# Optimization experiments

Hardware: AMD Instinct MI355X
Metric: run time of the kernel (lower is better)

Reference implementation:

```python
import jax, jax.numpy as jnp
import numpy as np

T, D, I, E, K = 2048, 2048, 5632, 8, 2


def setup_inputs() -> dict:
    key = jax.random.key(0)
    k1, k2, k3, k4, k5 = jax.random.split(key, 5)
    s = 0.02
    return {
        "x": jax.random.normal(k1, (T, D), dtype=jnp.float32),
        "gate_w": jax.random.normal(k2, (E, D), dtype=jnp.float32) * s,
        "w_gate": jax.random.normal(k3, (E, I, D), dtype=jnp.float32) * s,
        "w_up": jax.random.normal(k4, (E, I, D), dtype=jnp.float32) * s,
        "w_down": jax.random.normal(k5, (E, D, I), dtype=jnp.float32) * s,
    }


def reference(x, gate_w, w_gate, w_up, w_down):
    # Router: logits [T, E], top-k then softmax over the k selected logits
    logits = x @ gate_w.T
    top_vals, top_idx = jax.lax.top_k(logits, K)          # [T, K]
    rw = jax.nn.softmax(top_vals, axis=-1)                # [T, K]
    # Dense combine weights [T, E]: sum of routing weights over selected slots.
    # Mathematically identical to the per-(expert, slot) scatter-add in torch,
    # since duplicate selections of the same expert just sum their weights.
    combine = jnp.sum(jax.nn.one_hot(top_idx, E, dtype=x.dtype) * rw[..., None], axis=1)  # [T, E]
    # SwiGLU expert MLPs, batched over experts (grouped GEMM as dense einsum)
    g = jnp.einsum("td,eid->tei", x, w_gate)              # [T, E, I]
    u = jnp.einsum("td,eid->tei", x, w_up)                # [T, E, I]
    h = jax.nn.silu(g) * u                                 # [T, E, I]
    out_e = jnp.einsum("tei,edi->ted", h, w_down)         # [T, E, D]
    return jnp.einsum("ted,te->td", out_e, combine)       # [T, D]
```

## Files before the change

kernel.cpp:

```cpp
#include <hip/hip_runtime.h>
#include <hip/hip_bf16.h>
#include <stdint.h>

#define TTOK 2048
#define DDIM 2048
#define IDIM 5632
#define NEXP 8

typedef __attribute__((ext_vector_type(8))) short bf16x8;
typedef __attribute__((ext_vector_type(4))) float f32x4;
typedef __attribute__((ext_vector_type(8))) unsigned short u16x8;
typedef __attribute__((ext_vector_type(4))) unsigned short u16x4;

__device__ __forceinline__ unsigned short f2bf(float f) {
  union { float f; uint32_t u; } v; v.f = f;
  uint32_t u = v.u + 0x7fffu + ((v.u >> 16) & 1u);
  return (unsigned short)(u >> 16);
}

__device__ __forceinline__ uint32_t fbits(float f) {
  union { float f; uint32_t u; } v; v.f = f; return v.u;
}

__device__ __forceinline__ u16x8 cvt8t(float4 a, float4 b) {
  union { u16x8 v; uint32_t w[4]; } r;
  r.w[0] = __builtin_amdgcn_perm(fbits(a.y), fbits(a.x), 0x07060302);
  r.w[1] = __builtin_amdgcn_perm(fbits(a.w), fbits(a.z), 0x07060302);
  r.w[2] = __builtin_amdgcn_perm(fbits(b.y), fbits(b.x), 0x07060302);
  r.w[3] = __builtin_amdgcn_perm(fbits(b.w), fbits(b.z), 0x07060302);
  return r.v;
}

typedef __attribute__((address_space(3))) void lds_t;
typedef const __attribute__((address_space(1))) void gbl_t;
__device__ __forceinline__ void gload16(const void* g, void* l) {
  __builtin_amdgcn_global_load_lds((gbl_t*)g, (lds_t*)l, 16, 0, 0);
}

#define PIPE_BAR() asm volatile("s_waitcnt vmcnt(4) lgkmcnt(0)\n\ts_barrier" ::: "memory")

__global__ __launch_bounds__(256) void router_kernel(
    const float* __restrict__ x, const float* __restrict__ gw,
    unsigned short* __restrict__ xbf,
    int* __restrict__ cnt, int* __restrict__ slots, float* __restrict__ wts)
{
  const int lane = threadIdx.x & 63;
  const int t = (blockIdx.x * blockDim.x + threadIdx.x) >> 6;
  const float* xr = x + (size_t)t * DDIM;
  float acc[NEXP];
#pragma unroll
  for (int e = 0; e < NEXP; ++e) acc[e] = 0.f;
#pragma unroll
  for (int it = 0; it < DDIM / 256; ++it) {
    const int d = (it * 64 + lane) * 4;
    const float4 xv = *(const float4*)(xr + d);
    u16x4 xb; xb[0]=f2bf(xv.x); xb[1]=f2bf(xv.y); xb[2]=f2bf(xv.z); xb[3]=f2bf(xv.w);
    *(u16x4*)(xbf + (size_t)t * DDIM + d) = xb;
#pragma unroll
    for (int e = 0; e < NEXP; ++e) {
      const float4 gv = *(const float4*)(gw + (size_t)e * DDIM + d);
      acc[e] += xv.x*gv.x + xv.y*gv.y + xv.z*gv.z + xv.w*gv.w;
    }
  }
#pragma unroll
  for (int e = 0; e < NEXP; ++e) {
    float v = acc[e];
#pragma unroll
    for (int off = 32; off > 0; off >>= 1) v += __shfl_xor(v, off);
    acc[e] = v;
  }
  if (lane == 0) {
    int i0 = 0; float v0 = acc[0];
#pragma unroll
    for (int e = 1; e < NEXP; ++e) if (acc[e] > v0) { v0 = acc[e]; i0 = e; }
    int i1 = -1; float v1 = -3.4e38f;
#pragma unroll
    for (int e = 0; e < NEXP; ++e) { if (e == i0) continue; if (acc[e] > v1) { v1 = acc[e]; i1 = e; } }
    const float e1 = __expf(v1 - v0);
    const float w0 = 1.f / (1.f + e1);
    const float w1 = e1 / (1.f + e1);
    const int p0 = atomicAdd(&cnt[i0], 1);
    slots[i0 * TTOK + p0] = t * 2;     wts[i0 * TTOK + p0] = w0;
    const int p1 = atomicAdd(&cnt[i1], 1);
    slots[i1 * TTOK + p1] = t * 2 + 1; wts[i1 * TTOK + p1] = w1;
  }
}

__global__ void plan_kernel(const int* __restrict__ cnt,
                            int* __restrict__ tilemap, int* __restrict__ ntiles)
{
  if (threadIdx.x == 0 && blockIdx.x == 0) {
    int n = 0;
#pragma unroll
    for (int e = 0; e < NEXP; ++e) {
      const int nt = (cnt[e] + 127) >> 7;
      for (int m = 0; m < nt; ++m) tilemap[n++] = (e << 8) | m;
    }
    ntiles[0] = n;
  }
}


__global__ __launch_bounds__(512, 4) void gateup_kernel(
    const unsigned short* __restrict__ xbf,
    const float* __restrict__ wg, const float* __restrict__ wu,
    const int* __restrict__ cnt, const int* __restrict__ slots,
    const int* __restrict__ tilemap, const int* __restrict__ ntiles,
    unsigned short* __restrict__ h)
{
  const int flat = (blockIdx.x & 7) * 440 + (blockIdx.x >> 3);
  const int ti = flat % 40;
  if (ti >= ntiles[0]) return;
  const int em = tilemap[ti];
  const int e = em >> 8;
  const int mt = em & 255;
  const int n0 = (flat / 40) * 64;
  const int count = cnt[e];
  const int m0 = mt * 128;

  __shared__ unsigned short A[2][128][64];
  __shared__ unsigned short Bg[2][64][64];
  __shared__ unsigned short Bu[2][64][64];
  __shared__ int rslot[128];
  __shared__ int rtok[128];

  const int tid = threadIdx.x;
  const int lane = tid & 63;
  const int wid = tid >> 6;

  if (tid < 128) {
    const int idx = m0 + tid;
    const int safe = slots[e * TTOK + m0];
    const int s = (idx < count) ? slots[e * TTOK + idx] : safe;
    rslot[tid] = (idx < count) ? s : -1;
    rtok[tid] = s >> 1;
  }
  __syncthreads();

  const int aswz = ((lane & 7) ^ ((lane >> 3) & 7)) * 8;
  const unsigned short* aptr[2];
#pragma unroll
  for (int j = 0; j < 2; ++j) {
    const int arow = wid * 16 + j * 8 + (lane >> 3);
    aptr[j] = xbf + (size_t)rtok[arow] * DDIM + aswz;
  }

  const int mat = wid >> 2;
  unsigned short (*Bm)[64][64] = (mat == 0) ? Bg : Bu;
  const float* wsel = (mat == 0) ? wg : wu;

  const int tidm = tid & 255;
  const int brow = tidm >> 2;
  const int bcb = (tidm & 3) * 2;
  const int bswz = brow & 7;
  const float* msrc = wsel + (size_t)e * IDIM * DDIM + (size_t)(n0 + brow) * DDIM + bcb * 8;

  const int wr = (wid >> 1) & 1, wc = wid & 1;
  const int fr = lane & 15;
  const int kc = lane >> 4;
  const int rsw = fr & 7;

  f32x4 acc[4][2] = {};

  float4 P[4];
#pragma unroll
  for (int j = 0; j < 2; ++j) gload16(aptr[j], &A[0][wid * 16][0] + j * 512);
#pragma unroll
  for (int q = 0; q < 4; ++q) P[q] = *(const float4*)(msrc + q * 4);
#pragma unroll
  for (int qq = 0; qq < 2; ++qq)
    *(u16x8*)&Bm[0][brow][((bcb + qq) ^ bswz) * 8] = cvt8t(P[qq * 2], P[qq * 2 + 1]);
#pragma unroll
  for (int q = 0; q < 4; ++q) P[q] = *(const float4*)(msrc + 64 + q * 4);
  PIPE_BAR();

#pragma unroll 2
  for (int t = 0; t < 32; ++t) {
    const int cur = t & 1;
    const int kp  = (t + 1 <= 31) ? (t + 1) * 64 : 31 * 64;
    const int kp2 = (t + 2 <= 31) ? (t + 2) * 64 : 31 * 64;

#pragma unroll
    for (int j = 0; j < 2; ++j) gload16(aptr[j] + kp, &A[cur ^ 1][wid * 16][0] + j * 512);
    __builtin_amdgcn_sched_barrier(0);
#pragma unroll
    for (int qq = 0; qq < 2; ++qq)
      *(u16x8*)&Bm[cur ^ 1][brow][((bcb + qq) ^ bswz) * 8] = cvt8t(P[qq * 2], P[qq * 2 + 1]);
#pragma unroll
    for (int q = 0; q < 4; ++q) P[q] = *(const float4*)(msrc + kp2 + q * 4);
    __builtin_amdgcn_sched_barrier(0);

    __builtin_amdgcn_s_setprio(1);
#pragma unroll
    for (int kk = 0; kk < 2; ++kk) {
      bf16x8 a[4], b[2];
      const int cs = ((kk * 4 + kc) ^ rsw) * 8;
#pragma unroll
      for (int mf = 0; mf < 4; ++mf)
        a[mf] = *(const bf16x8*)&A[cur][wr * 64 + mf * 16 + fr][cs];
#pragma unroll
      for (int nf = 0; nf < 2; ++nf)
        b[nf] = *(const bf16x8*)&Bm[cur][wc * 32 + nf * 16 + fr][cs];
#pragma unroll
      for (int mf = 0; mf < 4; ++mf)
#pragma unroll
        for (int nf = 0; nf < 2; ++nf)
          acc[mf][nf] = __builtin_amdgcn_mfma_f32_16x16x32_bf16(a[mf], b[nf], acc[mf][nf], 0, 0, 0);
    }
    __builtin_amdgcn_s_setprio(0);

    PIPE_BAR();
  }

  __syncthreads();
  float* uex = (float*)&A[0][0][0];
  if (mat == 1) {
#pragma unroll
    for (int mf = 0; mf < 4; ++mf)
#pragma unroll
      for (int nf = 0; nf < 2; ++nf)
#pragma unroll
        for (int j = 0; j < 4; ++j) {
          const int r = wr * 64 + mf * 16 + (lane >> 4) * 4 + j;
          const int c = wc * 32 + nf * 16 + fr;
          uex[r * 64 + c] = acc[mf][nf][j];
        }
  }
  __syncthreads();
  if (mat == 0) {
#pragma unroll
    for (int mf = 0; mf < 4; ++mf)
#pragma unroll
      for (int nf = 0; nf < 2; ++nf)
#pragma unroll
        for (int j = 0; j < 4; ++j) {
          const int r = wr * 64 + mf * 16 + (lane >> 4) * 4 + j;
          const int c = wc * 32 + nf * 16 + fr;
          const int s = rslot[r];
          if (s >= 0) {
            const float g = acc[mf][nf][j];
            const float u = uex[r * 64 + c];
            const float hv = g / (1.f + __expf(-g)) * u;
            h[(size_t)s * IDIM + n0 + c] = f2bf(hv);
          }
        }
  }
}

__global__ __launch_bounds__(256, 4) void down_kernel(
    const unsigned short* __restrict__ h,
    const float* __restrict__ wd,
    const int* __restrict__ cnt, const int* __restrict__ slots,
    const float* __restrict__ wts,
    const int* __restrict__ tilemap, const int* __restrict__ ntiles,
    float* __restrict__ out)
{
  const int flat = (blockIdx.x & 7) * 320 + (blockIdx.x >> 3);
  const int ti = flat % 40;
  if (ti >= ntiles[0]) return;
  const int em = tilemap[ti];
  const int e = em >> 8;
  const int mt = em & 255;
  const int rest = flat / 40;
  const int n0 = (rest & 31) * 64;
  const int kbase = (rest >> 5) * (IDIM / 2);
  const int count = cnt[e];
  const int m0 = mt * 128;

  __shared__ unsigned short A[2][128][64];
  __shared__ unsigned short B[2][64][64];
  __shared__ int rslot[128];
  __shared__ float rw[128];

  const int tid = threadIdx.x;
  const int lane = tid & 63;
  const int wid = tid >> 6;

  if (tid < 128) {
    const int idx = m0 + tid;
    const int safe = slots[e * TTOK + m0];
    const int s = (idx < count) ? slots[e * TTOK + idx] : safe;
    rslot[tid] = (idx < count) ? s : (safe | 0x40000000);
    rw[tid] = (idx < count) ? wts[e * TTOK + idx] : 0.f;
  }
  __syncthreads();

  const int aswz = ((lane & 7) ^ ((lane >> 3) & 7)) * 8;
  const unsigned short* aptr[4];
#pragma unroll
  for (int j = 0; j < 4; ++j) {
    const int arow = wid * 32 + j * 8 + (lane >> 3);
    aptr[j] = h + (size_t)(rslot[arow] & 0x3fffffff) * IDIM + kbase + aswz;
  }

  const int brow = tid >> 2;
  const int bcb = (tid & 3) * 2;
  const int bswz = brow & 7;
  const float* bsrc = wd + (size_t)e * DDIM * IDIM + (size_t)(n0 + brow) * IDIM + kbase + bcb * 8;

  const int wr = wid >> 1, wc = wid & 1;
  const int fr = lane & 15;
  const int kc = lane >> 4;
  const int rsw = fr & 7;

  f32x4 acc[4][2] = {};

  float4 P[4];
#pragma unroll
  for (int j = 0; j < 4; ++j) gload16(aptr[j], &A[0][wid * 32][0] + j * 512);
#pragma unroll
  for (int q = 0; q < 4; ++q) P[q] = *(const float4*)(bsrc + q * 4);
#pragma unroll
  for (int qq = 0; qq < 2; ++qq)
    *(u16x8*)&B[0][brow][((bcb + qq) ^ bswz) * 8] = cvt8t(P[qq * 2], P[qq * 2 + 1]);
#pragma unroll
  for (int q = 0; q < 4; ++q) P[q] = *(const float4*)(bsrc + 64 + q * 4);
  asm volatile("s_waitcnt vmcnt(4) lgkmcnt(0)\n\ts_barrier" ::: "memory");

#pragma unroll 2
  for (int t = 0; t < 44; ++t) {
    const int cur = t & 1;
    const int kp  = (t + 1 <= 43) ? (t + 1) * 64 : 43 * 64;
    const int kp2 = (t + 2 <= 43) ? (t + 2) * 64 : 43 * 64;

#pragma unroll
    for (int j = 0; j < 4; ++j) gload16(aptr[j] + kp, &A[cur ^ 1][wid * 32][0] + j * 512);
    __builtin_amdgcn_sched_barrier(0);
#pragma unroll
    for (int qq = 0; qq < 2; ++qq)
      *(u16x8*)&B[cur ^ 1][brow][((bcb + qq) ^ bswz) * 8] = cvt8t(P[qq * 2], P[qq * 2 + 1]);
#pragma unroll
    for (int q = 0; q < 4; ++q) P[q] = *(const float4*)(bsrc + kp2 + q * 4);
    __builtin_amdgcn_sched_barrier(0);

    __builtin_amdgcn_s_setprio(1);
#pragma unroll
    for (int kk = 0; kk < 2; ++kk) {
      bf16x8 a[4], b[2];
      const int cs = ((kk * 4 + kc) ^ rsw) * 8;
#pragma unroll
      for (int mf = 0; mf < 4; ++mf)
        a[mf] = *(const bf16x8*)&A[cur][wr * 64 + mf * 16 + fr][cs];
#pragma unroll
      for (int nf = 0; nf < 2; ++nf)
        b[nf] = *(const bf16x8*)&B[cur][wc * 32 + nf * 16 + fr][cs];
#pragma unroll
      for (int mf = 0; mf < 4; ++mf)
#pragma unroll
        for (int nf = 0; nf < 2; ++nf)
          acc[mf][nf] = __builtin_amdgcn_mfma_f32_16x16x32_bf16(a[mf], b[nf], acc[mf][nf], 0, 0, 0);
    }
    __builtin_amdgcn_s_setprio(0);

    asm volatile("s_waitcnt vmcnt(4) lgkmcnt(0)\n\ts_barrier" ::: "memory");
  }

#pragma unroll
  for (int mf = 0; mf < 4; ++mf)
#pragma unroll
    for (int j = 0; j < 4; ++j) {
      const int r = wr * 64 + mf * 16 + (lane >> 4) * 4 + j;
      const int s = rslot[r];
      if (!(s & 0x40000000)) {
        const int t2 = s >> 1;
        const float w = rw[r];
#pragma unroll
        for (int nf = 0; nf < 2; ++nf)
          atomicAdd(out + (size_t)t2 * DDIM + n0 + wc * 32 + nf * 16 + fr,
                    acc[mf][nf][j] * w);
      }
    }
}

extern "C" void kernel_launch(void* const* d_in, const int* in_sizes, int n_in,
                              void* d_out, int out_size, void* d_ws, size_t ws_size,
                              hipStream_t stream) {
  const float* x  = (const float*)d_in[0];
  const float* gw = (const float*)d_in[1];
  const float* wg = (const float*)d_in[2];
  const float* wu = (const float*)d_in[3];
  const float* wd = (const float*)d_in[4];
  float* out = (float*)d_out;

  char* ws = (char*)d_ws;
  unsigned short* xbf = (unsigned short*)ws;
  unsigned short* h   = (unsigned short*)(ws + 8388608);
  int*   slots = (int*)(ws + 8388608 + 46137344);
  float* wts   = (float*)(ws + 8388608 + 46137344 + 65536);
  int*   cnt   = (int*)(ws + 8388608 + 46137344 + 131072);
  int*   tmap  = (int*)(ws + 8388608 + 46137344 + 131072 + 32);
  int*   ntl   = (int*)(ws + 8388608 + 46137344 + 131072 + 288);

  hipMemsetAsync(cnt, 0, NEXP * sizeof(int), stream);
  hipMemsetAsync(d_out, 0, (size_t)TTOK * DDIM * sizeof(float), stream);

  router_kernel<<<TTOK / 4, 256, 0, stream>>>(x, gw, xbf, cnt, slots, wts);
  plan_kernel<<<1, 64, 0, stream>>>(cnt, tmap, ntl);
  gateup_kernel<<<3520, 512, 0, stream>>>(xbf, wg, wu, cnt, slots, tmap, ntl, h);
  down_kernel<<<2560, 256, 0, stream>>>(h, wd, cnt, slots, wts, tmap, ntl, out);
}
```

Before: 806.6 us.

## Pack routed tokens per expert into contiguous bf16 buffer before grouped GEMMs

Adds a pack kernel that gathers each expert's routed tokens from x, converts them to bf16 and stores them contiguously in expert-sorted order, with zero-padded tail rows. Gate/up and down GEMMs now read A rows linearly from this buffer and the h buffer instead of through per-row slot indirection. This removes the gathered row loads, the slot lookup and its shared-memory sync in gateup. It also drops the s_setprio hints around the MFMA loops. The cost is an extra kernel launch and an extra pass writing the packed activations.

```diff
diff --git a/kernel.cpp b/kernel.cpp
--- a/kernel.cpp
+++ b/kernel.cpp
@@ -41,7 +41,6 @@
 
 __global__ __launch_bounds__(256) void router_kernel(
     const float* __restrict__ x, const float* __restrict__ gw,
-    unsigned short* __restrict__ xbf,
     int* __restrict__ cnt, int* __restrict__ slots, float* __restrict__ wts)
 {
   const int lane = threadIdx.x & 63;
@@ -54,8 +53,6 @@
   for (int it = 0; it < DDIM / 256; ++it) {
     const int d = (it * 64 + lane) * 4;
     const float4 xv = *(const float4*)(xr + d);
-    u16x4 xb; xb[0]=f2bf(xv.x); xb[1]=f2bf(xv.y); xb[2]=f2bf(xv.z); xb[3]=f2bf(xv.w);
-    *(u16x4*)(xbf + (size_t)t * DDIM + d) = xb;
 #pragma unroll
     for (int e = 0; e < NEXP; ++e) {
       const float4 gv = *(const float4*)(gw + (size_t)e * DDIM + d);
@@ -87,24 +84,55 @@
 }
 
 __global__ void plan_kernel(const int* __restrict__ cnt,
-                            int* __restrict__ tilemap, int* __restrict__ ntiles)
+                            int* __restrict__ tilemap, int* __restrict__ ntiles,
+                            int* __restrict__ po)
 {
   if (threadIdx.x == 0 && blockIdx.x == 0) {
-    int n = 0;
+    int n = 0, off = 0;
 #pragma unroll
     for (int e = 0; e < NEXP; ++e) {
+      po[e] = off;
       const int nt = (cnt[e] + 127) >> 7;
       for (int m = 0; m < nt; ++m) tilemap[n++] = (e << 8) | m;
+      off += nt << 7;
     }
     ntiles[0] = n;
   }
 }
 
+__global__ __launch_bounds__(256) void pack_kernel(
+    const float* __restrict__ x, const int* __restrict__ cnt,
+    const int* __restrict__ slots, const int* __restrict__ po,
+    unsigned short* __restrict__ xs)
+{
+  const int e = blockIdx.x >> 9;
+  const int count = cnt[e];
+  const int padded = (count + 127) & ~127;
+  const int rr = (blockIdx.x & 511) * 4 + (threadIdx.x >> 6);
+  if (rr >= padded) return;
+  const int lane = threadIdx.x & 63;
+  unsigned short* dst = xs + (size_t)(po[e] + rr) * DDIM;
+  if (rr < count) {
+    const float* src = x + (size_t)(slots[e * TTOK + rr] >> 1) * DDIM;
+#pragma unroll
+    for (int i = 0; i < 8; ++i) {
+      const int d = (i * 64 + lane) * 4;
+      const float4 v = *(const float4*)(src + d);
+      u16x4 b; b[0]=f2bf(v.x); b[1]=f2bf(v.y); b[2]=f2bf(v.z); b[3]=f2bf(v.w);
+      *(u16x4*)(dst + d) = b;
+    }
+  } else {
+    const u16x4 z = {};
+#pragma unroll
+    for (int i = 0; i < 8; ++i) *(u16x4*)(dst + (i * 64 + lane) * 4) = z;
+  }
+}
+
 
 __global__ __launch_bounds__(512, 4) void gateup_kernel(
-    const unsigned short* __restrict__ xbf,
+    const unsigned short* __restrict__ xs,
     const float* __restrict__ wg, const float* __restrict__ wu,
-    const int* __restrict__ cnt, const int* __restrict__ slots,
+    const int* __restrict__ cnt, const int* __restrict__ po,
     const int* __restrict__ tilemap, const int* __restrict__ ntiles,
     unsigned short* __restrict__ h)
 {
@@ -117,32 +145,22 @@
   const int n0 = (flat / 40) * 64;
   const int count = cnt[e];
   const int m0 = mt * 128;
+  const int abase = po[e] + m0;
 
   __shared__ unsigned short A[2][128][64];
   __shared__ unsigned short Bg[2][64][64];
   __shared__ unsigned short Bu[2][64][64];
-  __shared__ int rslot[128];
-  __shared__ int rtok[128];
 
   const int tid = threadIdx.x;
   const int lane = tid & 63;
   const int wid = tid >> 6;
 
-  if (tid < 128) {
-    const int idx = m0 + tid;
-    const int safe = slots[e * TTOK + m0];
-    const int s = (idx < count) ? slots[e * TTOK + idx] : safe;
-    rslot[tid] = (idx < count) ? s : -1;
-    rtok[tid] = s >> 1;
-  }
-  __syncthreads();
-
   const int aswz = ((lane & 7) ^ ((lane >> 3) & 7)) * 8;
   const unsigned short* aptr[2];
 #pragma unroll
   for (int j = 0; j < 2; ++j) {
     const int arow = wid * 16 + j * 8 + (lane >> 3);
-    aptr[j] = xbf + (size_t)rtok[arow] * DDIM + aswz;
+    aptr[j] = xs + (size_t)(abase + arow) * DDIM + aswz;
   }
 
   const int mat = wid >> 2;
@@ -190,7 +208,6 @@
     for (int q = 0; q < 4; ++q) P[q] = *(const float4*)(msrc + kp2 + q * 4);
     __builtin_amdgcn_sched_barrier(0);
 
-    __builtin_amdgcn_s_setprio(1);
 #pragma unroll
     for (int kk = 0; kk < 2; ++kk) {
       bf16x8 a[4], b[2];
@@ -207,7 +224,6 @@
         for (int nf = 0; nf < 2; ++nf)
           acc[mf][nf] = __builtin_amdgcn_mfma_f32_16x16x32_bf16(a[mf], b[nf], acc[mf][nf], 0, 0, 0);
     }
-    __builtin_amdgcn_s_setprio(0);
 
     PIPE_BAR();
   }
@@ -236,12 +252,11 @@
         for (int j = 0; j < 4; ++j) {
           const int r = wr * 64 + mf * 16 + (lane >> 4) * 4 + j;
           const int c = wc * 32 + nf * 16 + fr;
-          const int s = rslot[r];
-          if (s >= 0) {
+          if (m0 + r < count) {
             const float g = acc[mf][nf][j];
             const float u = uex[r * 64 + c];
             const float hv = g / (1.f + __expf(-g)) * u;
-            h[(size_t)s * IDIM + n0 + c] = f2bf(hv);
+            h[(size_t)(abase + r) * IDIM + n0 + c] = f2bf(hv);
           }
         }
   }
@@ -251,7 +266,7 @@
     const unsigned short* __restrict__ h,
     const float* __restrict__ wd,
     const int* __restrict__ cnt, const int* __restrict__ slots,
-    const float* __restrict__ wts,
+    const float* __restrict__ wts, const int* __restrict__ po,
     const int* __restrict__ tilemap, const int* __restrict__ ntiles,
     float* __restrict__ out)
 {
@@ -266,10 +281,11 @@
   const int kbase = (rest >> 5) * (IDIM / 2);
   const int count = cnt[e];
   const int m0 = mt * 128;
+  const int abase = po[e] + m0;
 
   __shared__ unsigned short A[2][128][64];
   __shared__ unsigned short B[2][64][64];
-  __shared__ int rslot[128];
+  __shared__ int rtok[128];
   __shared__ float rw[128];
 
   const int tid = threadIdx.x;
@@ -278,19 +294,16 @@
 
   if (tid < 128) {
     const int idx = m0 + tid;
-    const int safe = slots[e * TTOK + m0];
-    const int s = (idx < count) ? slots[e * TTOK + idx] : safe;
-    rslot[tid] = (idx < count) ? s : (safe | 0x40000000);
+    rtok[tid] = (idx < count) ? (slots[e * TTOK + idx] >> 1) : 0;
     rw[tid] = (idx < count) ? wts[e * TTOK + idx] : 0.f;
   }
-  __syncthreads();
 
   const int aswz = ((lane & 7) ^ ((lane >> 3) & 7)) * 8;
   const unsigned short* aptr[4];
 #pragma unroll
   for (int j = 0; j < 4; ++j) {
     const int arow = wid * 32 + j * 8 + (lane >> 3);
-    aptr[j] = h + (size_t)(rslot[arow] & 0x3fffffff) * IDIM + kbase + aswz;
+    aptr[j] = h + (size_t)(abase + arow) * IDIM + kbase + aswz;
   }
 
   const int brow = tid >> 2;
@@ -315,7 +328,7 @@
     *(u16x8*)&B[0][brow][((bcb + qq) ^ bswz) * 8] = cvt8t(P[qq * 2], P[qq * 2 + 1]);
 #pragma unroll
   for (int q = 0; q < 4; ++q) P[q] = *(const float4*)(bsrc + 64 + q * 4);
-  asm volatile("s_waitcnt vmcnt(4) lgkmcnt(0)\n\ts_barrier" ::: "memory");
+  PIPE_BAR();
 
 #pragma unroll 2
   for (int t = 0; t < 44; ++t) {
@@ -333,7 +346,6 @@
     for (int q = 0; q < 4; ++q) P[q] = *(const float4*)(bsrc + kp2 + q * 4);
     __builtin_amdgcn_sched_barrier(0);
 
-    __builtin_amdgcn_s_setprio(1);
 #pragma unroll
     for (int kk = 0; kk < 2; ++kk) {
       bf16x8 a[4], b[2];
@@ -350,9 +362,8 @@
         for (int nf = 0; nf < 2; ++nf)
           acc[mf][nf] = __builtin_amdgcn_mfma_f32_16x16x32_bf16(a[mf], b[nf], acc[mf][nf], 0, 0, 0);
     }
-    __builtin_amdgcn_s_setprio(0);
-
-    asm volatile("s_waitcnt vmcnt(4) lgkmcnt(0)\n\ts_barrier" ::: "memory");
+
+    PIPE_BAR();
   }
 
 #pragma unroll
@@ -360,9 +371,8 @@
 #pragma unroll
     for (int j = 0; j < 4; ++j) {
       const int r = wr * 64 + mf * 16 + (lane >> 4) * 4 + j;
-      const int s = rslot[r];
-      if (!(s & 0x40000000)) {
-        const int t2 = s >> 1;
+      if (m0 + r < count) {
+        const int t2 = rtok[r];
         const float w = rw[r];
 #pragma unroll
         for (int nf = 0; nf < 2; ++nf)
@@ -383,19 +393,21 @@
   float* out = (float*)d_out;
 
   char* ws = (char*)d_ws;
-  unsigned short* xbf = (unsigned short*)ws;
-  unsigned short* h   = (unsigned short*)(ws + 8388608);
-  int*   slots = (int*)(ws + 8388608 + 46137344);
-  float* wts   = (float*)(ws + 8388608 + 46137344 + 65536);
-  int*   cnt   = (int*)(ws + 8388608 + 46137344 + 131072);
-  int*   tmap  = (int*)(ws + 8388608 + 46137344 + 131072 + 32);
-  int*   ntl   = (int*)(ws + 8388608 + 46137344 + 131072 + 288);
+  unsigned short* xs = (unsigned short*)ws;
+  unsigned short* h  = (unsigned short*)(ws + 20971520);
+  int*   slots = (int*)(ws + 78643200);
+  float* wts   = (float*)(ws + 78708736);
+  int*   cnt   = (int*)(ws + 78774272);
+  int*   tmap  = (int*)(ws + 78774304);
+  int*   ntl   = (int*)(ws + 78774560);
+  int*   po    = (int*)(ws + 78774564);
 
   hipMemsetAsync(cnt, 0, NEXP * sizeof(int), stream);
   hipMemsetAsync(d_out, 0, (size_t)TTOK * DDIM * sizeof(float), stream);
 
-  router_kernel<<<TTOK / 4, 256, 0, stream>>>(x, gw, xbf, cnt, slots, wts);
-  plan_kernel<<<1, 64, 0, stream>>>(cnt, tmap, ntl);
-  gateup_kernel<<<3520, 512, 0, stream>>>(xbf, wg, wu, cnt, slots, tmap, ntl, h);
-  down_kernel<<<2560, 256, 0, stream>>>(h, wd, cnt, slots, wts, tmap, ntl, out);
-}
+  router_kernel<<<TTOK / 4, 256, 0, stream>>>(x, gw, cnt, slots, wts);
+  plan_kernel<<<1, 64, 0, stream>>>(cnt, tmap, ntl, po);
+  pack_kernel<<<NEXP * 512, 256, 0, stream>>>(x, cnt, slots, po, xs);
+  gateup_kernel<<<3520, 512, 0, stream>>>(xs, wg, wu, cnt, po, tmap, ntl, h);
+  down_kernel<<<2560, 256, 0, stream>>>(h, wd, cnt, slots, wts, po, tmap, ntl, out);
+}
```

Result: slower. 849.0 us (+5.3%).

## Load weight fragments directly into registers and compact h by expert

Applied to the files above, without the earlier changes.

Both GEMM kernels stop staging the fp32 weights through LDS. Each lane now loads exactly the weight elements its MFMA B-fragment needs, converts them to bf16 in registers, and prefetches one step ahead. The plan kernel computes per-expert padded row offsets, so h is written and read in a contiguous expert-sorted layout instead of being scattered by slot index. The down kernel moves to 512 threads with 16-column wave slices. This removes LDS write traffic and bank pressure for B, but waves that share columns now load the same weights redundantly from global memory and cache. Padded rows of the compacted h may also read past the buffer's logical extent.

```diff
diff --git a/kernel.cpp b/kernel.cpp
--- a/kernel.cpp
+++ b/kernel.cpp
@@ -36,8 +36,6 @@
 __device__ __forceinline__ void gload16(const void* g, void* l) {
   __builtin_amdgcn_global_load_lds((gbl_t*)g, (lds_t*)l, 16, 0, 0);
 }
-
-#define PIPE_BAR() asm volatile("s_waitcnt vmcnt(4) lgkmcnt(0)\n\ts_barrier" ::: "memory")
 
 __global__ __launch_bounds__(256) void router_kernel(
     const float* __restrict__ x, const float* __restrict__ gw,
@@ -87,14 +85,17 @@
 }
 
 __global__ void plan_kernel(const int* __restrict__ cnt,
-                            int* __restrict__ tilemap, int* __restrict__ ntiles)
+                            int* __restrict__ tilemap, int* __restrict__ ntiles,
+                            int* __restrict__ po)
 {
   if (threadIdx.x == 0 && blockIdx.x == 0) {
-    int n = 0;
+    int n = 0, off = 0;
 #pragma unroll
     for (int e = 0; e < NEXP; ++e) {
+      po[e] = off;
       const int nt = (cnt[e] + 127) >> 7;
       for (int m = 0; m < nt; ++m) tilemap[n++] = (e << 8) | m;
+      off += nt << 7;
     }
     ntiles[0] = n;
   }
@@ -105,6 +106,7 @@
     const unsigned short* __restrict__ xbf,
     const float* __restrict__ wg, const float* __restrict__ wu,
     const int* __restrict__ cnt, const int* __restrict__ slots,
+    const int* __restrict__ po,
     const int* __restrict__ tilemap, const int* __restrict__ ntiles,
     unsigned short* __restrict__ h)
 {
@@ -117,11 +119,9 @@
   const int n0 = (flat / 40) * 64;
   const int count = cnt[e];
   const int m0 = mt * 128;
+  const int abase = po[e] + m0;
 
   __shared__ unsigned short A[2][128][64];
-  __shared__ unsigned short Bg[2][64][64];
-  __shared__ unsigned short Bu[2][64][64];
-  __shared__ int rslot[128];
   __shared__ int rtok[128];
 
   const int tid = threadIdx.x;
@@ -130,86 +130,75 @@
 
   if (tid < 128) {
     const int idx = m0 + tid;
-    const int safe = slots[e * TTOK + m0];
-    const int s = (idx < count) ? slots[e * TTOK + idx] : safe;
-    rslot[tid] = (idx < count) ? s : -1;
-    rtok[tid] = s >> 1;
+    rtok[tid] = (idx < count) ? (slots[e * TTOK + idx] >> 1) : (slots[e * TTOK + m0] >> 1);
   }
   __syncthreads();
 
   const int aswz = ((lane & 7) ^ ((lane >> 3) & 7)) * 8;
-  const unsigned short* aptr[2];
-#pragma unroll
-  for (int j = 0; j < 2; ++j) {
-    const int arow = wid * 16 + j * 8 + (lane >> 3);
-    aptr[j] = xbf + (size_t)rtok[arow] * DDIM + aswz;
-  }
-
+  const unsigned short* ap0 = xbf + (size_t)rtok[wid * 16     + (lane >> 3)] * DDIM + aswz;
+  const unsigned short* ap1 = xbf + (size_t)rtok[wid * 16 + 8 + (lane >> 3)] * DDIM + aswz;
+
+  const int wr  = wid & 1;
+  const int wc  = (wid >> 1) & 1;
   const int mat = wid >> 2;
-  unsigned short (*Bm)[64][64] = (mat == 0) ? Bg : Bu;
   const float* wsel = (mat == 0) ? wg : wu;
 
-  const int tidm = tid & 255;
-  const int brow = tidm >> 2;
-  const int bcb = (tidm & 3) * 2;
-  const int bswz = brow & 7;
-  const float* msrc = wsel + (size_t)e * IDIM * DDIM + (size_t)(n0 + brow) * DDIM + bcb * 8;
-
-  const int wr = (wid >> 1) & 1, wc = wid & 1;
   const int fr = lane & 15;
+  const int kq = (lane >> 4) * 8;
+  const float* bp0 = wsel + (size_t)e * IDIM * DDIM + (size_t)(n0 + wc * 32 +      fr) * DDIM + kq;
+  const float* bp1 = wsel + (size_t)e * IDIM * DDIM + (size_t)(n0 + wc * 32 + 16 + fr) * DDIM + kq;
+
   const int kc = lane >> 4;
   const int rsw = fr & 7;
 
   f32x4 acc[4][2] = {};
-
-  float4 P[4];
-#pragma unroll
-  for (int j = 0; j < 2; ++j) gload16(aptr[j], &A[0][wid * 16][0] + j * 512);
-#pragma unroll
-  for (int q = 0; q < 4; ++q) P[q] = *(const float4*)(msrc + q * 4);
-#pragma unroll
-  for (int qq = 0; qq < 2; ++qq)
-    *(u16x8*)&Bm[0][brow][((bcb + qq) ^ bswz) * 8] = cvt8t(P[qq * 2], P[qq * 2 + 1]);
-#pragma unroll
-  for (int q = 0; q < 4; ++q) P[q] = *(const float4*)(msrc + 64 + q * 4);
-  PIPE_BAR();
+  float4 Brg[8];
+
+  gload16(ap0, &A[0][wid * 16][0]);
+  gload16(ap1, &A[0][wid * 16 + 8][0]);
+  __builtin_amdgcn_sched_barrier(0);
+  Brg[0] = *(const float4*)(bp0);        Brg[1] = *(const float4*)(bp0 + 4);
+  Brg[2] = *(const float4*)(bp1);        Brg[3] = *(const float4*)(bp1 + 4);
+  Brg[4] = *(const float4*)(bp0 + 32);   Brg[5] = *(const float4*)(bp0 + 36);
+  Brg[6] = *(const float4*)(bp1 + 32);   Brg[7] = *(const float4*)(bp1 + 36);
+  asm volatile("s_waitcnt vmcnt(8) lgkmcnt(0)\n\ts_barrier" ::: "memory");
 
 #pragma unroll 2
   for (int t = 0; t < 32; ++t) {
     const int cur = t & 1;
-    const int kp  = (t + 1 <= 31) ? (t + 1) * 64 : 31 * 64;
-    const int kp2 = (t + 2 <= 31) ? (t + 2) * 64 : 31 * 64;
-
-#pragma unroll
-    for (int j = 0; j < 2; ++j) gload16(aptr[j] + kp, &A[cur ^ 1][wid * 16][0] + j * 512);
+    const int kp = ((t + 1 < 32) ? t + 1 : 31) * 64;
+
+    gload16(ap0 + kp, &A[cur ^ 1][wid * 16][0]);
+    gload16(ap1 + kp, &A[cur ^ 1][wid * 16 + 8][0]);
     __builtin_amdgcn_sched_barrier(0);
-#pragma unroll
-    for (int qq = 0; qq < 2; ++qq)
-      *(u16x8*)&Bm[cur ^ 1][brow][((bcb + qq) ^ bswz) * 8] = cvt8t(P[qq * 2], P[qq * 2 + 1]);
-#pragma unroll
-    for (int q = 0; q < 4; ++q) P[q] = *(const float4*)(msrc + kp2 + q * 4);
-    __builtin_amdgcn_sched_barrier(0);
-
-    __builtin_amdgcn_s_setprio(1);
+
+    bf16x8 bfr[4];
+#pragma unroll
+    for (int f = 0; f < 4; ++f)
+      bfr[f] = (bf16x8)cvt8t(Brg[2 * f], Brg[2 * f + 1]);
+
+    Brg[0] = *(const float4*)(bp0 + kp);        Brg[1] = *(const float4*)(bp0 + kp + 4);
+    Brg[2] = *(const float4*)(bp1 + kp);        Brg[3] = *(const float4*)(bp1 + kp + 4);
+    Brg[4] = *(const float4*)(bp0 + kp + 32);   Brg[5] = *(const float4*)(bp0 + kp + 36);
+    Brg[6] = *(const float4*)(bp1 + kp);        Brg[6] = *(const float4*)(bp1 + kp + 32);
+    Brg[7] = *(const float4*)(bp1 + kp + 36);
+
 #pragma unroll
     for (int kk = 0; kk < 2; ++kk) {
-      bf16x8 a[4], b[2];
       const int cs = ((kk * 4 + kc) ^ rsw) * 8;
+      bf16x8 a[4];
 #pragma unroll
       for (int mf = 0; mf < 4; ++mf)
         a[mf] = *(const bf16x8*)&A[cur][wr * 64 + mf * 16 + fr][cs];
 #pragma unroll
-      for (int nf = 0; nf < 2; ++nf)
-        b[nf] = *(const bf16x8*)&Bm[cur][wc * 32 + nf * 16 + fr][cs];
-#pragma unroll
       for (int mf = 0; mf < 4; ++mf)
 #pragma unroll
         for (int nf = 0; nf < 2; ++nf)
-          acc[mf][nf] = __builtin_amdgcn_mfma_f32_16x16x32_bf16(a[mf], b[nf], acc[mf][nf], 0, 0, 0);
-    }
-    __builtin_amdgcn_s_setprio(0);
-
-    PIPE_BAR();
+          acc[mf][nf] = __builtin_amdgcn_mfma_f32_16x16x32_bf16(
+              a[mf], bfr[kk * 2 + nf], acc[mf][nf], 0, 0, 0);
+    }
+
+    asm volatile("s_waitcnt vmcnt(8) lgkmcnt(0)\n\ts_barrier" ::: "memory");
   }
 
   __syncthreads();
@@ -222,8 +211,7 @@
 #pragma unroll
         for (int j = 0; j < 4; ++j) {
           const int r = wr * 64 + mf * 16 + (lane >> 4) * 4 + j;
-          const int c = wc * 32 + nf * 16 + fr;
-          uex[r * 64 + c] = acc[mf][nf][j];
+          uex[r * 64 + wc * 32 + nf * 16 + fr] = acc[mf][nf][j];
         }
   }
   __syncthreads();
@@ -235,23 +223,22 @@
 #pragma unroll
         for (int j = 0; j < 4; ++j) {
           const int r = wr * 64 + mf * 16 + (lane >> 4) * 4 + j;
-          const int c = wc * 32 + nf * 16 + fr;
-          const int s = rslot[r];
-          if (s >= 0) {
+          if (m0 + r < count) {
+            const int c = wc * 32 + nf * 16 + fr;
             const float g = acc[mf][nf][j];
             const float u = uex[r * 64 + c];
             const float hv = g / (1.f + __expf(-g)) * u;
-            h[(size_t)s * IDIM + n0 + c] = f2bf(hv);
+            h[(size_t)(abase + r) * IDIM + n0 + c] = f2bf(hv);
           }
         }
   }
 }
 
-__global__ __launch_bounds__(256, 4) void down_kernel(
-    const unsigned short* __restrict__ h,
+__global__ __launch_bounds__(512, 4) void down_kernel(
+    const unsigned short* __restrict__ hb,
     const float* __restrict__ wd,
     const int* __restrict__ cnt, const int* __restrict__ slots,
-    const float* __restrict__ wts,
+    const float* __restrict__ wts, const int* __restrict__ po,
     const int* __restrict__ tilemap, const int* __restrict__ ntiles,
     float* __restrict__ out)
 {
@@ -266,10 +253,10 @@
   const int kbase = (rest >> 5) * (IDIM / 2);
   const int count = cnt[e];
   const int m0 = mt * 128;
+  const int abase = po[e] + m0;
 
   __shared__ unsigned short A[2][128][64];
-  __shared__ unsigned short B[2][64][64];
-  __shared__ int rslot[128];
+  __shared__ int rtok[128];
   __shared__ float rw[128];
 
   const int tid = threadIdx.x;
@@ -278,79 +265,61 @@
 
   if (tid < 128) {
     const int idx = m0 + tid;
-    const int safe = slots[e * TTOK + m0];
-    const int s = (idx < count) ? slots[e * TTOK + idx] : safe;
-    rslot[tid] = (idx < count) ? s : (safe | 0x40000000);
+    rtok[tid] = (idx < count) ? (slots[e * TTOK + idx] >> 1) : 0;
     rw[tid] = (idx < count) ? wts[e * TTOK + idx] : 0.f;
   }
   __syncthreads();
 
   const int aswz = ((lane & 7) ^ ((lane >> 3) & 7)) * 8;
-  const unsigned short* aptr[4];
-#pragma unroll
-  for (int j = 0; j < 4; ++j) {
-    const int arow = wid * 32 + j * 8 + (lane >> 3);
-    aptr[j] = h + (size_t)(rslot[arow] & 0x3fffffff) * IDIM + kbase + aswz;
-  }
-
-  const int brow = tid >> 2;
-  const int bcb = (tid & 3) * 2;
-  const int bswz = brow & 7;
-  const float* bsrc = wd + (size_t)e * DDIM * IDIM + (size_t)(n0 + brow) * IDIM + kbase + bcb * 8;
-
-  const int wr = wid >> 1, wc = wid & 1;
+  const unsigned short* ap0 = hb + (size_t)(abase + wid * 16     + (lane >> 3)) * IDIM + kbase + aswz;
+  const unsigned short* ap1 = hb + (size_t)(abase + wid * 16 + 8 + (lane >> 3)) * IDIM + kbase + aswz;
+
+  const int wr = wid & 1;
+  const int wc = wid >> 1;
   const int fr = lane & 15;
+  const int kq = (lane >> 4) * 8;
+  const float* bp = wd + (size_t)e * DDIM * IDIM + (size_t)(n0 + wc * 16 + fr) * IDIM + kbase + kq;
+
   const int kc = lane >> 4;
   const int rsw = fr & 7;
 
-  f32x4 acc[4][2] = {};
-
-  float4 P[4];
-#pragma unroll
-  for (int j = 0; j < 4; ++j) gload16(aptr[j], &A[0][wid * 32][0] + j * 512);
-#pragma unroll
-  for (int q = 0; q < 4; ++q) P[q] = *(const float4*)(bsrc + q * 4);
-#pragma unroll
-  for (int qq = 0; qq < 2; ++qq)
-    *(u16x8*)&B[0][brow][((bcb + qq) ^ bswz) * 8] = cvt8t(P[qq * 2], P[qq * 2 + 1]);
-#pragma unroll
-  for (int q = 0; q < 4; ++q) P[q] = *(const float4*)(bsrc + 64 + q * 4);
+  f32x4 acc[4] = {};
+  float4 Brg[4];
+
+  gload16(ap0, &A[0][wid * 16][0]);
+  gload16(ap1, &A[0][wid * 16 + 8][0]);
+  __builtin_amdgcn_sched_barrier(0);
+  Brg[0] = *(const float4*)(bp);        Brg[1] = *(const float4*)(bp + 4);
+  Brg[2] = *(const float4*)(bp + 32);   Brg[3] = *(const float4*)(bp + 36);
   asm volatile("s_waitcnt vmcnt(4) lgkmcnt(0)\n\ts_barrier" ::: "memory");
 
 #pragma unroll 2
   for (int t = 0; t < 44; ++t) {
     const int cur = t & 1;
-    const int kp  = (t + 1 <= 43) ? (t + 1) * 64 : 43 * 64;
-    const int kp2 = (t + 2 <= 43) ? (t + 2) * 64 : 43 * 64;
-
-#pragma unroll
-    for (int j = 0; j < 4; ++j) gload16(aptr[j] + kp, &A[cur ^ 1][wid * 32][0] + j * 512);
+    const int kp = ((t + 1 < 44) ? t + 1 : 43) * 64;
+
+    gload16(ap0 + kp, &A[cur ^ 1][wid * 16][0]);
+    gload16(ap1 + kp, &A[cur ^ 1][wid * 16 + 8][0]);
     __builtin_amdgcn_sched_barrier(0);
-#pragma unroll
-    for (int qq = 0; qq < 2; ++qq)
-      *(u16x8*)&B[cur ^ 1][brow][((bcb + qq) ^ bswz) * 8] = cvt8t(P[qq * 2], P[qq * 2 + 1]);
-#pragma unroll
-    for (int q = 0; q < 4; ++q) P[q] = *(const float4*)(bsrc + kp2 + q * 4);
-    __builtin_amdgcn_sched_barrier(0);
-
-    __builtin_amdgcn_s_setprio(1);
+
+    bf16x8 bfr[2];
+    bfr[0] = (bf16x8)cvt8t(Brg[0], Brg[1]);
+    bfr[1] = (bf16x8)cvt8t(Brg[2], Brg[3]);
+
+    Brg[0] = *(const float4*)(bp + kp);        Brg[1] = *(const float4*)(bp + kp + 4);
+    Brg[2] = *(const float4*)(bp + kp + 32);   Brg[3] = *(const float4*)(bp + kp + 36);
+
 #pragma unroll
     for (int kk = 0; kk < 2; ++kk) {
-      bf16x8 a[4], b[2];
       const int cs = ((kk * 4 + kc) ^ rsw) * 8;
+      bf16x8 a[4];
 #pragma unroll
       for (int mf = 0; mf < 4; ++mf)
         a[mf] = *(const bf16x8*)&A[cur][wr * 64 + mf * 16 + fr][cs];
 #pragma unroll
-      for (int nf = 0; nf < 2; ++nf)
-        b[nf] = *(const bf16x8*)&B[cur][wc * 32 + nf * 16 + fr][cs];
-#pragma unroll
       for (int mf = 0; mf < 4; ++mf)
-#pragma unroll
-        for (int nf = 0; nf < 2; ++nf)
-          acc[mf][nf] = __builtin_amdgcn_mfma_f32_16x16x32_bf16(a[mf], b[nf], acc[mf][nf], 0, 0, 0);
-    }
-    __builtin_amdgcn_s_setprio(0);
+        acc[mf] = __builtin_amdgcn_mfma_f32_16x16x32_bf16(a[mf], bfr[kk], acc[mf], 0, 0, 0);
+    }
 
     asm volatile("s_waitcnt vmcnt(4) lgkmcnt(0)\n\ts_barrier" ::: "memory");
   }
@@ -360,14 +329,9 @@
 #pragma unroll
     for (int j = 0; j < 4; ++j) {
       const int r = wr * 64 + mf * 16 + (lane >> 4) * 4 + j;
-      const int s = rslot[r];
-      if (!(s & 0x40000000)) {
-        const int t2 = s >> 1;
-        const float w = rw[r];
-#pragma unroll
-        for (int nf = 0; nf < 2; ++nf)
-          atomicAdd(out + (size_t)t2 * DDIM + n0 + wc * 32 + nf * 16 + fr,
-                    acc[mf][nf][j] * w);
+      if (m0 + r < count) {
+        atomicAdd(out + (size_t)rtok[r] * DDIM + n0 + wc * 16 + fr,
+                  acc[mf][j] * rw[r]);
       }
     }
 }
@@ -385,17 +349,18 @@
   char* ws = (char*)d_ws;
   unsigned short* xbf = (unsigned short*)ws;
   unsigned short* h   = (unsigned short*)(ws + 8388608);
-  int*   slots = (int*)(ws + 8388608 + 46137344);
-  float* wts   = (float*)(ws + 8388608 + 46137344 + 65536);
-  int*   cnt   = (int*)(ws + 8388608 + 46137344 + 131072);
-  int*   tmap  = (int*)(ws + 8388608 + 46137344 + 131072 + 32);
-  int*   ntl   = (int*)(ws + 8388608 + 46137344 + 131072 + 288);
+  int*   slots = (int*)(ws + 66060288);
+  float* wts   = (float*)(ws + 66125824);
+  int*   cnt   = (int*)(ws + 66191360);
+  int*   tmap  = (int*)(ws + 66191392);
+  int*   ntl   = (int*)(ws + 66191648);
+  int*   po    = (int*)(ws + 66191652);
 
   hipMemsetAsync(cnt, 0, NEXP * sizeof(int), stream);
   hipMemsetAsync(d_out, 0, (size_t)TTOK * DDIM * sizeof(float), stream);
 
   router_kernel<<<TTOK / 4, 256, 0, stream>>>(x, gw, xbf, cnt, slots, wts);
-  plan_kernel<<<1, 64, 0, stream>>>(cnt, tmap, ntl);
-  gateup_kernel<<<3520, 512, 0, stream>>>(xbf, wg, wu, cnt, slots, tmap, ntl, h);
-  down_kernel<<<2560, 256, 0, stream>>>(h, wd, cnt, slots, wts, tmap, ntl, out);
-}
+  plan_kernel<<<1, 64, 0, stream>>>(cnt, tmap, ntl, po);
+  gateup_kernel<<<3520, 512, 0, stream>>>(xbf, wg, wu, cnt, slots, po, tmap, ntl, h);
+  down_kernel<<<2560, 512, 0, stream>>>(h, wd, cnt, slots, wts, po, tmap, ntl, out);
+}
```

New measurement: 1.457 ms. 80.6% more time.

## Stage fp32 down-proj weights directly to LDS and convert to bf16 at MFMA read

Applied to the files above, without the earlier changes.

The down kernel now async-copies fp32 w_down tiles straight into a swizzled fp32 LDS buffer with gload16, instead of loading to registers, converting to bf16 and writing to LDS with a two-stage register prefetch. Conversion to bf16 moves to the point where each wave reads B fragments before the MFMAs. The goal is to cut VGPR pressure and register staging, letting the DMA path overlap loads. The cost is doubled LDS use for B, repeated conversion by each reading wave, and prefetch depth dropping from two stages to one. The gate/up kernel also swaps its wave-to-row/column mapping.

```diff
diff --git a/kernel.cpp b/kernel.cpp
--- a/kernel.cpp
+++ b/kernel.cpp
@@ -155,7 +155,8 @@
   const int bswz = brow & 7;
   const float* msrc = wsel + (size_t)e * IDIM * DDIM + (size_t)(n0 + brow) * DDIM + bcb * 8;
 
-  const int wr = (wid >> 1) & 1, wc = wid & 1;
+  const int wr = wid & 1;
+  const int wc = (wid >> 1) & 1;
   const int fr = lane & 15;
   const int kc = lane >> 4;
   const int rsw = fr & 7;
@@ -222,8 +223,7 @@
 #pragma unroll
         for (int j = 0; j < 4; ++j) {
           const int r = wr * 64 + mf * 16 + (lane >> 4) * 4 + j;
-          const int c = wc * 32 + nf * 16 + fr;
-          uex[r * 64 + c] = acc[mf][nf][j];
+          uex[r * 64 + wc * 32 + nf * 16 + fr] = acc[mf][nf][j];
         }
   }
   __syncthreads();
@@ -235,9 +235,9 @@
 #pragma unroll
         for (int j = 0; j < 4; ++j) {
           const int r = wr * 64 + mf * 16 + (lane >> 4) * 4 + j;
-          const int c = wc * 32 + nf * 16 + fr;
           const int s = rslot[r];
           if (s >= 0) {
+            const int c = wc * 32 + nf * 16 + fr;
             const float g = acc[mf][nf][j];
             const float u = uex[r * 64 + c];
             const float hv = g / (1.f + __expf(-g)) * u;
@@ -268,7 +268,7 @@
   const int m0 = mt * 128;
 
   __shared__ unsigned short A[2][128][64];
-  __shared__ unsigned short B[2][64][64];
+  __shared__ float Bf[2][64][64];
   __shared__ int rslot[128];
   __shared__ float rw[128];
 
@@ -293,10 +293,13 @@
     aptr[j] = h + (size_t)(rslot[arow] & 0x3fffffff) * IDIM + kbase + aswz;
   }
 
-  const int brow = tid >> 2;
-  const int bcb = (tid & 3) * 2;
-  const int bswz = brow & 7;
-  const float* bsrc = wd + (size_t)e * DDIM * IDIM + (size_t)(n0 + brow) * IDIM + kbase + bcb * 8;
+  const float* bptr[4];
+#pragma unroll
+  for (int g = 0; g < 4; ++g) {
+    const int brow = wid * 16 + g * 4 + (lane >> 4);
+    const int bch = (lane & 15) ^ (brow & 15);
+    bptr[g] = wd + (size_t)e * DDIM * IDIM + (size_t)(n0 + brow) * IDIM + kbase + bch * 4;
+  }
 
   const int wr = wid >> 1, wc = wid & 1;
   const int fr = lane & 15;
@@ -305,54 +308,47 @@
 
   f32x4 acc[4][2] = {};
 
-  float4 P[4];
 #pragma unroll
   for (int j = 0; j < 4; ++j) gload16(aptr[j], &A[0][wid * 32][0] + j * 512);
 #pragma unroll
-  for (int q = 0; q < 4; ++q) P[q] = *(const float4*)(bsrc + q * 4);
-#pragma unroll
-  for (int qq = 0; qq < 2; ++qq)
-    *(u16x8*)&B[0][brow][((bcb + qq) ^ bswz) * 8] = cvt8t(P[qq * 2], P[qq * 2 + 1]);
-#pragma unroll
-  for (int q = 0; q < 4; ++q) P[q] = *(const float4*)(bsrc + 64 + q * 4);
-  asm volatile("s_waitcnt vmcnt(4) lgkmcnt(0)\n\ts_barrier" ::: "memory");
+  for (int g = 0; g < 4; ++g) gload16(bptr[g], &Bf[0][wid * 16 + g * 4][0]);
+  __syncthreads();
 
 #pragma unroll 2
   for (int t = 0; t < 44; ++t) {
     const int cur = t & 1;
-    const int kp  = (t + 1 <= 43) ? (t + 1) * 64 : 43 * 64;
-    const int kp2 = (t + 2 <= 43) ? (t + 2) * 64 : 43 * 64;
-
-#pragma unroll
-    for (int j = 0; j < 4; ++j) gload16(aptr[j] + kp, &A[cur ^ 1][wid * 32][0] + j * 512);
+    if (t < 43) {
+      const int kp = (t + 1) * 64;
+#pragma unroll
+      for (int j = 0; j < 4; ++j) gload16(aptr[j] + kp, &A[cur ^ 1][wid * 32][0] + j * 512);
+#pragma unroll
+      for (int g = 0; g < 4; ++g) gload16(bptr[g] + kp, &Bf[cur ^ 1][wid * 16 + g * 4][0]);
+    }
     __builtin_amdgcn_sched_barrier(0);
-#pragma unroll
-    for (int qq = 0; qq < 2; ++qq)
-      *(u16x8*)&B[cur ^ 1][brow][((bcb + qq) ^ bswz) * 8] = cvt8t(P[qq * 2], P[qq * 2 + 1]);
-#pragma unroll
-    for (int q = 0; q < 4; ++q) P[q] = *(const float4*)(bsrc + kp2 + q * 4);
-    __builtin_amdgcn_sched_barrier(0);
 
     __builtin_amdgcn_s_setprio(1);
 #pragma unroll
     for (int kk = 0; kk < 2; ++kk) {
-      bf16x8 a[4], b[2];
       const int cs = ((kk * 4 + kc) ^ rsw) * 8;
+      bf16x8 a[4];
 #pragma unroll
       for (int mf = 0; mf < 4; ++mf)
         a[mf] = *(const bf16x8*)&A[cur][wr * 64 + mf * 16 + fr][cs];
 #pragma unroll
-      for (int nf = 0; nf < 2; ++nf)
-        b[nf] = *(const bf16x8*)&B[cur][wc * 32 + nf * 16 + fr][cs];
-#pragma unroll
-      for (int mf = 0; mf < 4; ++mf)
-#pragma unroll
-        for (int nf = 0; nf < 2; ++nf)
-          acc[mf][nf] = __builtin_amdgcn_mfma_f32_16x16x32_bf16(a[mf], b[nf], acc[mf][nf], 0, 0, 0);
+      for (int nf = 0; nf < 2; ++nf) {
+        const int br = wc * 32 + nf * 16 + fr;
+        const int c0 = kk * 8 + kc * 2;
+        const float4 fa = *(const float4*)&Bf[cur][br][(c0 ^ fr) * 4];
+        const float4 fb = *(const float4*)&Bf[cur][br][((c0 + 1) ^ fr) * 4];
+        const bf16x8 b = (bf16x8)cvt8t(fa, fb);
+#pragma unroll
+        for (int mf = 0; mf < 4; ++mf)
+          acc[mf][nf] = __builtin_amdgcn_mfma_f32_16x16x32_bf16(a[mf], b, acc[mf][nf], 0, 0, 0);
+      }
     }
     __builtin_amdgcn_s_setprio(0);
 
-    asm volatile("s_waitcnt vmcnt(4) lgkmcnt(0)\n\ts_barrier" ::: "memory");
+    __syncthreads();
   }
 
 #pragma unroll
```

Result: faster. 788.9 us (-2.2%).
